# Kernel optimization log

Measured on AMD Instinct MI355X. Metric: run time of the kernel, lower is better.

The kernel has to match this reference:

```python
import jax, jax.numpy as jnp
import numpy as np

B, T, D, H = 64, 512, 512, 1024


def setup_inputs() -> dict:
    key = jax.random.key(0)
    k_x, k_m, k_wi, k_wh = jax.random.split(key, 4)
    x = jax.random.normal(k_x, (B, T, D), dtype=jnp.float32)
    mask = jax.random.randint(k_m, (B, T), 0, 2, dtype=jnp.int32)
    # LSTMCell params: xavier_uniform for W_ih, orthogonal for W_hh, zero biases
    lim = float(np.sqrt(6.0 / (4 * H + D)))
    W_ih = jax.random.uniform(k_wi, (4 * H, D), dtype=jnp.float32, minval=-lim, maxval=lim)
    A = jax.random.normal(k_wh, (4 * H, H), dtype=jnp.float32)
    Q, _ = jnp.linalg.qr(A.T)  # (H, 4H) columns orthonormal -> rows of W_hh orthogonal-ish per torch init
    W_hh = Q.T.astype(jnp.float32)
    W_hh = jnp.concatenate([W_hh] * ((4 * H) // W_hh.shape[0]), axis=0)[: 4 * H]
    b_ih = jnp.zeros((4 * H,), dtype=jnp.float32)
    b_hh = jnp.zeros((4 * H,), dtype=jnp.float32)
    h0 = jnp.zeros((1, H), dtype=jnp.float32)
    c0 = jnp.zeros((1, H), dtype=jnp.float32)
    return {"x": x, "mask": mask, "W_ih": W_ih, "W_hh": W_hh,
            "b_ih": b_ih, "b_hh": b_hh, "h0": h0, "c0": c0}


def reference(x, mask, W_ih, W_hh, b_ih, b_hh, h0, c0):
    Bn, Tn, _ = x.shape
    Hn = h0.shape[1]
    # Precompute input projection for all timesteps: (B, T, 4H)
    xg = jnp.einsum('btd,gd->btg', x, W_ih) + b_ih + b_hh

    def step(carry, inp):
        h, c = carry
        xg_t, m_t = inp  # (B, 4H), (B,)
        gates = xg_t + h @ W_hh.T  # (B, 4H)
        i, f, g, o = jnp.split(gates, 4, axis=-1)  # torch LSTMCell gate order i,f,g,o
        i = jax.nn.sigmoid(i)
        f = jax.nn.sigmoid(f)
        g = jnp.tanh(g)
        o = jax.nn.sigmoid(o)
        c_new = f * c + i * g
        h_new = o * jnp.tanh(c_new)
        keep = (m_t != 0)[:, None]
        h2 = jnp.where(keep, h_new, h)
        c2 = jnp.where(keep, c_new, c)
        return (h2, c2), h2

    h_init = jnp.broadcast_to(h0, (Bn, Hn))
    c_init = jnp.broadcast_to(c0, (Bn, Hn))
    xs = (jnp.swapaxes(xg, 0, 1), mask.T)  # time-major for scan
    (_, _), hs = jax.lax.scan(step, (h_init, c_init), xs)
    return jnp.swapaxes(hs, 0, 1)  # (B, T, H)
```

## Files before the change

### kernel.cpp

```cpp
#include <hip/hip_runtime.h>

#define B_   64
#define T_   512
#define D_   512
#define H_   1024
#define G4   4096
#define KTOT 1536
#define KC_N 48
#define AP   1544

typedef float f32x4 __attribute__((ext_vector_type(4)));
typedef short s16x8 __attribute__((ext_vector_type(8)));

__device__ __forceinline__ unsigned short f2bf(float f) {
    unsigned int u = __float_as_uint(f);
    u = (u + 0x7fffu + ((u >> 16) & 1u)) >> 16;
    return (unsigned short)u;
}
__device__ __forceinline__ float bf2f(unsigned short h) {
    return __uint_as_float(((unsigned int)h) << 16);
}
__device__ __forceinline__ float sigm(float x) { return 1.f / (1.f + __expf(-x)); }
__device__ __forceinline__ float tanh_f(float x) { return 1.f - 2.f / (__expf(2.f * x) + 1.f); }

__global__ __launch_bounds__(256) void pack_w(const float* __restrict__ W_ih,
                                              const float* __restrict__ W_hh,
                                              unsigned short* __restrict__ Wpk) {
    int tid = blockIdx.x * 256 + threadIdx.x;
    int j    = tid & 7;
    int lane = (tid >> 3) & 63;
    int rest = tid >> 9;
    int kc = rest % KC_N;
    int c  = rest / KC_N;
    int npk = c * 16 + (lane & 15);
    int jh = npk >> 2, g = npk & 3;
    int row = g * H_ + jh;
    int k = kc * 32 + (lane >> 4) * 8 + j;
    float v = (k < D_) ? W_ih[row * D_ + k] : W_hh[row * H_ + (k - D_)];
    Wpk[tid] = f2bf(v);
}

__global__ __launch_bounds__(256) void init_state(const float* __restrict__ h0,
                                                  const float* __restrict__ c0,
                                                  const float* __restrict__ b_ih,
                                                  const float* __restrict__ b_hh,
                                                  unsigned short* __restrict__ h_a,
                                                  float* __restrict__ c_cur,
                                                  float* __restrict__ bias_p) {
    int tid = blockIdx.x * 256 + threadIdx.x;
    int j = tid & (H_ - 1);
    h_a[tid]  = f2bf(h0[j]);
    c_cur[tid] = c0[j];
    if (tid < G4) {
        int jh = tid >> 2, g = tid & 3;
        bias_p[tid] = b_ih[g * H_ + jh] + b_hh[g * H_ + jh];
    }
}

__global__ __launch_bounds__(256) void lstm_step(
    const float* __restrict__ x, const int* __restrict__ mask,
    const unsigned short* __restrict__ Wpk, const float* __restrict__ bias_p,
    const unsigned short* __restrict__ h_in, unsigned short* __restrict__ h_out,
    float* __restrict__ c_cur, float* __restrict__ out, int t)
{
    __shared__ unsigned short At[16 * AP];
    __shared__ float Dl[16][66];

    const int tid = threadIdx.x;
    const int b0 = blockIdx.y * 16;
    const int bx = blockIdx.x;

    #pragma unroll
    for (int i = 0; i < 8; ++i) {
        int e = i * 256 + tid;
        int r = e >> 7, c4 = e & 127;
        float4 v = *reinterpret_cast<const float4*>(x + ((b0 + r) * T_ + t) * D_ + c4 * 4);
        unsigned int lo = ((unsigned int)f2bf(v.y) << 16) | f2bf(v.x);
        unsigned int hi = ((unsigned int)f2bf(v.w) << 16) | f2bf(v.z);
        *reinterpret_cast<uint2*>(&At[r * AP + c4 * 4]) = make_uint2(lo, hi);
    }
    #pragma unroll
    for (int i = 0; i < 8; ++i) {
        int e = i * 256 + tid;
        int r = e >> 7, c8 = e & 127;
        uint4 v = *reinterpret_cast<const uint4*>(h_in + (b0 + r) * H_ + c8 * 8);
        *reinterpret_cast<uint4*>(&At[r * AP + D_ + c8 * 8]) = v;
    }
    __syncthreads();

    const int w = tid >> 6, l = tid & 63;
    const int quad = l >> 4, l15 = l & 15;
    const int cgrp = bx * 4 + w;

    f32x4 acc = {0.f, 0.f, 0.f, 0.f};
    const unsigned short* atp = &At[l15 * AP + quad * 8];
    const unsigned short* bp  = Wpk + ((size_t)(cgrp * KC_N) * 64 + l) * 8;
    #pragma unroll 4
    for (int kc = 0; kc < KC_N; ++kc) {
        s16x8 af = *reinterpret_cast<const s16x8*>(atp + kc * 32);
        s16x8 bf = *reinterpret_cast<const s16x8*>(bp + kc * 64 * 8);
        acc = __builtin_amdgcn_mfma_f32_16x16x32_bf16(af, bf, acc, 0, 0, 0);
    }
    #pragma unroll
    for (int r = 0; r < 4; ++r)
        Dl[quad * 4 + r][w * 16 + l15] = acc[r];
    __syncthreads();

    const int b = tid >> 4, u = tid & 15;
    const int jh = bx * 16 + u;
    float4 bias = *reinterpret_cast<const float4*>(bias_p + bx * 64 + u * 4);
    float gi = sigm (Dl[b][u * 4 + 0] + bias.x);
    float gf = sigm (Dl[b][u * 4 + 1] + bias.y);
    float gg = tanh_f(Dl[b][u * 4 + 2] + bias.z);
    float go = sigm (Dl[b][u * 4 + 3] + bias.w);

    const int sidx = (b0 + b) * H_ + jh;
    float c_old = c_cur[sidx];
    float h_old = bf2f(At[b * AP + D_ + jh]);
    float c_new = gf * c_old + gi * gg;
    float h_new = go * tanh_f(c_new);
    int m = mask[(b0 + b) * T_ + t];
    float h2 = m ? h_new : h_old;
    float c2 = m ? c_new : c_old;
    c_cur[sidx] = c2;
    h_out[sidx] = f2bf(h2);
    out[((size_t)(b0 + b) * T_ + t) * H_ + jh] = h2;
}

extern "C" void kernel_launch(void* const* d_in, const int* in_sizes, int n_in,
                              void* d_out, int out_size, void* d_ws, size_t ws_size,
                              hipStream_t stream)
{
    const float* x    = (const float*)d_in[0];
    const int*   mask = (const int*)d_in[1];
    const float* W_ih = (const float*)d_in[2];
    const float* W_hh = (const float*)d_in[3];
    const float* b_ih = (const float*)d_in[4];
    const float* b_hh = (const float*)d_in[5];
    const float* h0   = (const float*)d_in[6];
    const float* c0   = (const float*)d_in[7];
    float* out = (float*)d_out;

    char* wsb = (char*)d_ws;
    unsigned short* Wpk    = (unsigned short*)(wsb);
    float*          bias_p = (float*)(wsb + 12582912);
    unsigned short* h_a    = (unsigned short*)(wsb + 12599296);
    unsigned short* h_b    = (unsigned short*)(wsb + 12730368);
    float*          c_cur  = (float*)(wsb + 12861440);

    pack_w<<<24576, 256, 0, stream>>>(W_ih, W_hh, Wpk);
    init_state<<<256, 256, 0, stream>>>(h0, c0, b_ih, b_hh, h_a, c_cur, bias_p);

    dim3 grid(64, 4);
    for (int t = 0; t < T_; ++t) {
        const unsigned short* hin = (t & 1) ? h_b : h_a;
        unsigned short*      hout = (t & 1) ? h_a : h_b;
        lstm_step<<<grid, 256, 0, stream>>>(x, mask, Wpk, bias_p, hin, hout, c_cur, out, t);
    }
}
```

Baseline: 3.436 ms.

## Replace per-timestep launches with a persistent LSTM kernel using flag barriers

Swaps the 512 per-timestep kernel launches for one persistent kernel of 256 blocks that loops over time. Each block loads its weight slice into registers once and keeps its cell state in registers. Blocks in the same batch group sync between steps through per-block flags in global memory, using release/acquire fences. The MFMA reduction is also split across four independent accumulators to shorten the dependency chain. The risks are that all 256 blocks must be resident at the same time or the kernel deadlocks, and that holding the weights needs very many VGPRs.

```diff
diff --git a/kernel.cpp b/kernel.cpp
--- a/kernel.cpp
+++ b/kernel.cpp
@@ -41,90 +41,128 @@
 }
 
 __global__ __launch_bounds__(256) void init_state(const float* __restrict__ h0,
-                                                  const float* __restrict__ c0,
                                                   const float* __restrict__ b_ih,
                                                   const float* __restrict__ b_hh,
                                                   unsigned short* __restrict__ h_a,
-                                                  float* __restrict__ c_cur,
-                                                  float* __restrict__ bias_p) {
+                                                  float* __restrict__ bias_p,
+                                                  int* __restrict__ bar) {
     int tid = blockIdx.x * 256 + threadIdx.x;
     int j = tid & (H_ - 1);
-    h_a[tid]  = f2bf(h0[j]);
-    c_cur[tid] = c0[j];
+    h_a[tid] = f2bf(h0[j]);
     if (tid < G4) {
         int jh = tid >> 2, g = tid & 3;
         bias_p[tid] = b_ih[g * H_ + jh] + b_hh[g * H_ + jh];
     }
+    if (tid < 4 * 64 * 16) bar[tid] = 0;
 }
 
-__global__ __launch_bounds__(256) void lstm_step(
+__global__ __launch_bounds__(256, 1) void lstm_persist(
     const float* __restrict__ x, const int* __restrict__ mask,
     const unsigned short* __restrict__ Wpk, const float* __restrict__ bias_p,
-    const unsigned short* __restrict__ h_in, unsigned short* __restrict__ h_out,
-    float* __restrict__ c_cur, float* __restrict__ out, int t)
+    const float* __restrict__ c0,
+    unsigned short* __restrict__ h_a, unsigned short* __restrict__ h_b,
+    float* __restrict__ out, int* __restrict__ bar)
 {
     __shared__ unsigned short At[16 * AP];
     __shared__ float Dl[16][66];
 
     const int tid = threadIdx.x;
-    const int b0 = blockIdx.y * 16;
-    const int bx = blockIdx.x;
-
-    #pragma unroll
-    for (int i = 0; i < 8; ++i) {
-        int e = i * 256 + tid;
-        int r = e >> 7, c4 = e & 127;
-        float4 v = *reinterpret_cast<const float4*>(x + ((b0 + r) * T_ + t) * D_ + c4 * 4);
-        unsigned int lo = ((unsigned int)f2bf(v.y) << 16) | f2bf(v.x);
-        unsigned int hi = ((unsigned int)f2bf(v.w) << 16) | f2bf(v.z);
-        *reinterpret_cast<uint2*>(&At[r * AP + c4 * 4]) = make_uint2(lo, hi);
-    }
-    #pragma unroll
-    for (int i = 0; i < 8; ++i) {
-        int e = i * 256 + tid;
-        int r = e >> 7, c8 = e & 127;
-        uint4 v = *reinterpret_cast<const uint4*>(h_in + (b0 + r) * H_ + c8 * 8);
-        *reinterpret_cast<uint4*>(&At[r * AP + D_ + c8 * 8]) = v;
-    }
-    __syncthreads();
-
+    const int blk = blockIdx.x;
+    const int bg  = blk & 3;
+    const int bxc = blk >> 2;
+    const int b0  = bg * 16;
     const int w = tid >> 6, l = tid & 63;
     const int quad = l >> 4, l15 = l & 15;
-    const int cgrp = bx * 4 + w;
+    const int cgrp = bxc * 4 + w;
 
-    f32x4 acc = {0.f, 0.f, 0.f, 0.f};
-    const unsigned short* atp = &At[l15 * AP + quad * 8];
-    const unsigned short* bp  = Wpk + ((size_t)(cgrp * KC_N) * 64 + l) * 8;
-    #pragma unroll 4
-    for (int kc = 0; kc < KC_N; ++kc) {
-        s16x8 af = *reinterpret_cast<const s16x8*>(atp + kc * 32);
-        s16x8 bf = *reinterpret_cast<const s16x8*>(bp + kc * 64 * 8);
-        acc = __builtin_amdgcn_mfma_f32_16x16x32_bf16(af, bf, acc, 0, 0, 0);
+    s16x8 wf[KC_N];
+    const unsigned short* wbase = Wpk + ((size_t)cgrp * KC_N * 64 + l) * 8;
+    #pragma unroll
+    for (int kc = 0; kc < KC_N; ++kc)
+        wf[kc] = *reinterpret_cast<const s16x8*>(wbase + (size_t)kc * 64 * 8);
+
+    const int eb = tid >> 4, eu = tid & 15;
+    const int jh = bxc * 16 + eu;
+    const float4 bias = *reinterpret_cast<const float4*>(bias_p + bxc * 64 + eu * 4);
+    const size_t sidx = (size_t)(b0 + eb) * H_ + jh;
+    float c_val = c0[jh];
+
+    int* slots = bar + bg * 64 * 16;
+
+    for (int t = 0; t < T_; ++t) {
+        const unsigned short* hin = (t & 1) ? h_b : h_a;
+        unsigned short*      hout = (t & 1) ? h_a : h_b;
+
+        const int m = mask[(b0 + eb) * T_ + t];
+
+        #pragma unroll
+        for (int i = 0; i < 8; ++i) {
+            int e = i * 256 + tid;
+            int r = e >> 7, c4 = e & 127;
+            float4 v = *reinterpret_cast<const float4*>(
+                x + ((size_t)(b0 + r) * T_ + t) * D_ + c4 * 4);
+            unsigned int lo = ((unsigned int)f2bf(v.y) << 16) | f2bf(v.x);
+            unsigned int hi = ((unsigned int)f2bf(v.w) << 16) | f2bf(v.z);
+            *reinterpret_cast<uint2*>(&At[r * AP + c4 * 4]) = make_uint2(lo, hi);
+        }
+
+        if (t > 0) {
+            if (tid < 64) {
+                while (__hip_atomic_load(&slots[tid * 16], __ATOMIC_RELAXED,
+                                         __HIP_MEMORY_SCOPE_AGENT) < t)
+                    __builtin_amdgcn_s_sleep(1);
+            }
+            __syncthreads();
+            __builtin_amdgcn_fence(__ATOMIC_ACQUIRE, "agent");
+        }
+
+        #pragma unroll
+        for (int i = 0; i < 8; ++i) {
+            int e = i * 256 + tid;
+            int r = e >> 7, c8 = e & 127;
+            uint4 v = *reinterpret_cast<const uint4*>(hin + (size_t)(b0 + r) * H_ + c8 * 8);
+            *reinterpret_cast<uint4*>(&At[r * AP + D_ + c8 * 8]) = v;
+        }
+        __syncthreads();
+
+        f32x4 acc0 = {0.f,0.f,0.f,0.f}, acc1 = {0.f,0.f,0.f,0.f};
+        f32x4 acc2 = {0.f,0.f,0.f,0.f}, acc3 = {0.f,0.f,0.f,0.f};
+        const unsigned short* atp = &At[l15 * AP + quad * 8];
+        #pragma unroll
+        for (int kc = 0; kc < KC_N; kc += 4) {
+            s16x8 a0 = *reinterpret_cast<const s16x8*>(atp + (kc + 0) * 32);
+            s16x8 a1 = *reinterpret_cast<const s16x8*>(atp + (kc + 1) * 32);
+            s16x8 a2 = *reinterpret_cast<const s16x8*>(atp + (kc + 2) * 32);
+            s16x8 a3 = *reinterpret_cast<const s16x8*>(atp + (kc + 3) * 32);
+            acc0 = __builtin_amdgcn_mfma_f32_16x16x32_bf16(a0, wf[kc + 0], acc0, 0, 0, 0);
+            acc1 = __builtin_amdgcn_mfma_f32_16x16x32_bf16(a1, wf[kc + 1], acc1, 0, 0, 0);
+            acc2 = __builtin_amdgcn_mfma_f32_16x16x32_bf16(a2, wf[kc + 2], acc2, 0, 0, 0);
+            acc3 = __builtin_amdgcn_mfma_f32_16x16x32_bf16(a3, wf[kc + 3], acc3, 0, 0, 0);
+        }
+        f32x4 accs = (acc0 + acc1) + (acc2 + acc3);
+        #pragma unroll
+        for (int r = 0; r < 4; ++r)
+            Dl[quad * 4 + r][w * 16 + l15] = accs[r];
+        __syncthreads();
+
+        float gi = sigm  (Dl[eb][eu * 4 + 0] + bias.x);
+        float gf = sigm  (Dl[eb][eu * 4 + 1] + bias.y);
+        float gg = tanh_f(Dl[eb][eu * 4 + 2] + bias.z);
+        float go = sigm  (Dl[eb][eu * 4 + 3] + bias.w);
+        float h_old = bf2f(At[eb * AP + D_ + jh]);
+        float c_new = gf * c_val + gi * gg;
+        float h_new = go * tanh_f(c_new);
+        float h2 = m ? h_new : h_old;
+        c_val    = m ? c_new : c_val;
+        hout[sidx] = f2bf(h2);
+        out[((size_t)(b0 + eb) * T_ + t) * H_ + jh] = h2;
+
+        __builtin_amdgcn_fence(__ATOMIC_RELEASE, "agent");
+        __syncthreads();
+        if (tid == 0)
+            __hip_atomic_store(&slots[bxc * 16], t + 1, __ATOMIC_RELAXED,
+                               __HIP_MEMORY_SCOPE_AGENT);
     }
-    #pragma unroll
-    for (int r = 0; r < 4; ++r)
-        Dl[quad * 4 + r][w * 16 + l15] = acc[r];
-    __syncthreads();
-
-    const int b = tid >> 4, u = tid & 15;
-    const int jh = bx * 16 + u;
-    float4 bias = *reinterpret_cast<const float4*>(bias_p + bx * 64 + u * 4);
-    float gi = sigm (Dl[b][u * 4 + 0] + bias.x);
-    float gf = sigm (Dl[b][u * 4 + 1] + bias.y);
-    float gg = tanh_f(Dl[b][u * 4 + 2] + bias.z);
-    float go = sigm (Dl[b][u * 4 + 3] + bias.w);
-
-    const int sidx = (b0 + b) * H_ + jh;
-    float c_old = c_cur[sidx];
-    float h_old = bf2f(At[b * AP + D_ + jh]);
-    float c_new = gf * c_old + gi * gg;
-    float h_new = go * tanh_f(c_new);
-    int m = mask[(b0 + b) * T_ + t];
-    float h2 = m ? h_new : h_old;
-    float c2 = m ? c_new : c_old;
-    c_cur[sidx] = c2;
-    h_out[sidx] = f2bf(h2);
-    out[((size_t)(b0 + b) * T_ + t) * H_ + jh] = h2;
 }
 
 extern "C" void kernel_launch(void* const* d_in, const int* in_sizes, int n_in,
@@ -146,15 +184,11 @@
     float*          bias_p = (float*)(wsb + 12582912);
     unsigned short* h_a    = (unsigned short*)(wsb + 12599296);
     unsigned short* h_b    = (unsigned short*)(wsb + 12730368);
-    float*          c_cur  = (float*)(wsb + 12861440);
+    int*            bar    = (int*)(wsb + 12861440);
 
     pack_w<<<24576, 256, 0, stream>>>(W_ih, W_hh, Wpk);
-    init_state<<<256, 256, 0, stream>>>(h0, c0, b_ih, b_hh, h_a, c_cur, bias_p);
+    init_state<<<256, 256, 0, stream>>>(h0, b_ih, b_hh, h_a, bias_p, bar);
 
-    dim3 grid(64, 4);
-    for (int t = 0; t < T_; ++t) {
-        const unsigned short* hin = (t & 1) ? h_b : h_a;
-        unsigned short*      hout = (t & 1) ? h_a : h_b;
-        lstm_step<<<grid, 256, 0, stream>>>(x, mask, Wpk, bias_p, hin, hout, c_cur, out, t);
-    }
+    lstm_persist<<<dim3(256), dim3(256), 0, stream>>>(
+        x, mask, Wpk, bias_p, c0, h_a, h_b, out, bar);
 }
```

New measurement: 13.53 ms. 3.94x slower.
